# Kernel optimization log

Measured on AMD Instinct MI355X. Metric: run time of the kernel, lower is better.

## Reference

```python
import jax, jax.numpy as jnp
import numpy as np
from jax import lax

EPS = 1e-5


def setup_inputs() -> dict:
    key = jax.random.key(0)
    ks = jax.random.split(key, 8)
    b, c_in, h, w = 16, 256, 64, 64
    c_out, kh, n_exp = 512, 3, 8
    fan_in = c_in * kh * kh
    bound_w = float(np.sqrt(6.0 / fan_in))  # kaiming_uniform a=sqrt(5) -> U(-sqrt(6/fan_in), +)
    bound_b = float(1.0 / np.sqrt(fan_in))
    return {
        "x": jax.random.normal(ks[0], (b, c_in, h, w), dtype=jnp.float32),
        "expert_weight": jax.random.uniform(ks[1], (n_exp, c_out, c_in, kh, kh), jnp.float32, -bound_w, bound_w),
        "expert_bias": jax.random.uniform(ks[2], (n_exp, c_out), jnp.float32, -bound_b, bound_b),
        "fc_w": jax.random.uniform(ks[3], (n_exp, c_in), jnp.float32, -1.0 / np.sqrt(c_in), 1.0 / np.sqrt(c_in)),
        "fc_b": jax.random.uniform(ks[4], (n_exp,), jnp.float32, -1.0 / np.sqrt(c_in), 1.0 / np.sqrt(c_in)),
        "bn_gamma": jnp.ones((c_out,), jnp.float32),
        "bn_beta": jnp.zeros((c_out,), jnp.float32),
    }


def reference(x, expert_weight, expert_bias, fc_w, fc_b, bn_gamma, bn_beta):
    # --- route_func: GAP -> Linear -> sigmoid -> (b, k) ---
    pooled = x.mean(axis=(2, 3))                       # (b, c_in)
    routing = jax.nn.sigmoid(pooled @ fc_w.T + fc_b)   # (b, k)

    # --- per-sample combined kernels and biases ---
    comb_w = jnp.einsum('bk,koihw->boihw', routing, expert_weight)  # (b, c_out, c_in, kh, kw)
    comb_b = routing @ expert_bias                                  # (b, c_out)

    # --- per-sample conv (equivalent of groups=b grouped conv) ---
    def conv_one(xi, wi):
        # xi: (c_in, h, w), wi: (c_out, c_in, kh, kw)
        return lax.conv_general_dilated(
            xi[None], wi, window_strides=(1, 1), padding=[(1, 1), (1, 1)],
            rhs_dilation=(1, 1), dimension_numbers=('NCHW', 'OIHW', 'NCHW'))[0]

    out = jax.vmap(conv_one)(x, comb_w) + comb_b[:, :, None, None]  # (b, c_out, h, w)

    # --- BatchNorm2d (training mode: batch statistics) ---
    mean = out.mean(axis=(0, 2, 3))
    var = out.var(axis=(0, 2, 3))
    out = (out - mean[None, :, None, None]) * (bn_gamma * lax.rsqrt(var + EPS))[None, :, None, None] \
          + bn_beta[None, :, None, None]

    # --- LeakyReLU(0.1) ---
    return jnp.where(out > 0, out, 0.1 * out)
```

## Files before the change

### kernel.cpp

```cpp
#include <hip/hip_runtime.h>
#include <hip/hip_bf16.h>
#include <stdint.h>

typedef unsigned short u16;
typedef short bf16x8 __attribute__((ext_vector_type(8)));
typedef float f32x4 __attribute__((ext_vector_type(4)));
typedef u16 u16x8 __attribute__((ext_vector_type(8)));

#define DEVFN static __device__ __forceinline__

#define NB 16
#define CIN 256
#define HH 64
#define WW 64
#define COUT 512
#define NPX 4096
#define NSTEP 72

DEVFN u16 bf16_rne(float f){
  union { float f; uint32_t u; } v; v.f = f;
  uint32_t u = v.u;
  return (u16)((u + 0x7fffu + ((u >> 16) & 1u)) >> 16);
}

DEVFN void gload16(const void* g, void* l){
  __builtin_amdgcn_global_load_lds((const __attribute__((address_space(1))) void*)g,
                                   (__attribute__((address_space(3))) void*)l,
                                   16, 0, 0);
}

#define VMWAIT(N) asm volatile("s_waitcnt vmcnt(" #N ")" ::: "memory")
#define BARRIER() do { __builtin_amdgcn_s_barrier(); \
                       __builtin_amdgcn_sched_barrier(0); \
                       asm volatile("" ::: "memory"); } while(0)

__global__ void k_route(const float* __restrict__ pooled, const float* __restrict__ fcw,
                        const float* __restrict__ fcb, float* __restrict__ routing){
  int bk = blockIdx.x;
  int b = bk >> 3, k = bk & 7;
  int l = threadIdx.x;
  float4 pv = ((const float4*)(pooled + b*CIN))[l];
  float4 wv = ((const float4*)(fcw   + k*CIN))[l];
  float s = pv.x*wv.x + pv.y*wv.y + pv.z*wv.z + pv.w*wv.w;
  for (int o = 32; o; o >>= 1) s += __shfl_down(s, o);
  if (l == 0) routing[b*8 + k] = 1.0f / (1.0f + __expf(-(s * (1.0f/(float)NPX) + fcb[k])));
}

__global__ void k_cbias(const float* __restrict__ routing, const float* __restrict__ eb,
                        float* __restrict__ cbias){
  int idx = blockIdx.x*256 + threadIdx.x;
  int b = idx >> 9, co = idx & 511;
  float s = 0.f;
  for (int k = 0; k < 8; k++) s += routing[b*8+k] * eb[k*COUT + co];
  cbias[idx] = s;
}

__global__ void k_wcomb(const float* __restrict__ routing, const float* __restrict__ ew,
                        u16* __restrict__ wc){
  int blk  = blockIdx.x;
  int step = blk >> 6;
  int cog  = blk & 63;
  int cb = step / 9, rs = step - cb*9;
  int t = threadIdx.x;
  int ci = t & 31, co = cog*8 + (t >> 5);
  int cig = cb*32 + ci;
  float wv[8];
#pragma unroll
  for (int k = 0; k < 8; k++)
    wv[k] = ew[(size_t)((k*COUT + co)*CIN + cig)*9 + rs];
  for (int b = 0; b < NB; b++){
    float s = 0.f;
#pragma unroll
    for (int k = 0; k < 8; k++) s += routing[b*8+k] * wv[k];
    wc[((size_t)(b*NSTEP + step)*COUT + co)*32 + ci] = bf16_rne(s);
  }
}

__global__ void k_xprep(const float* __restrict__ x, u16* __restrict__ xt,
                        float* __restrict__ pooled){
  int blk = blockIdx.x;
  int ctile = blk & 3;
  int h = (blk >> 2) & 63;
  int b = blk >> 8;
  __shared__ u16 S[64][66];
  int t = threadIdx.x;
  {
    int ci_l = t >> 2, w0 = (t & 3) * 16;
    const float4* src = (const float4*)(x + ((size_t)((b*CIN + ctile*64 + ci_l)*HH + h)*WW + w0));
    float4 a = src[0], bb = src[1], c = src[2], d = src[3];
    u16* row = &S[ci_l][w0];
    row[0]=bf16_rne(a.x);  row[1]=bf16_rne(a.y);  row[2]=bf16_rne(a.z);  row[3]=bf16_rne(a.w);
    row[4]=bf16_rne(bb.x); row[5]=bf16_rne(bb.y); row[6]=bf16_rne(bb.z); row[7]=bf16_rne(bb.w);
    row[8]=bf16_rne(c.x);  row[9]=bf16_rne(c.y);  row[10]=bf16_rne(c.z); row[11]=bf16_rne(c.w);
    row[12]=bf16_rne(d.x); row[13]=bf16_rne(d.y); row[14]=bf16_rne(d.z); row[15]=bf16_rne(d.w);
    float s = a.x+a.y+a.z+a.w + bb.x+bb.y+bb.z+bb.w + c.x+c.y+c.z+c.w + d.x+d.y+d.z+d.w;
    s += __shfl_down(s, 2);
    s += __shfl_down(s, 1);
    if ((t & 3) == 0) atomicAdd(&pooled[b*CIN + ctile*64 + ci_l], s);
  }
  __syncthreads();
  {
    int w_l = t >> 2, cig = (t & 3) * 16;
    u16x8 v0, v1;
#pragma unroll
    for (int j = 0; j < 8; j++){ v0[j] = S[cig+j][w_l]; v1[j] = S[cig+8+j][w_l]; }
    u16* dst = xt + ((size_t)(b*66 + h + 1)*68 + (w_l + 1))*CIN + ctile*64 + cig;
    *(u16x8*)(dst)     = v0;
    *(u16x8*)(dst + 8) = v1;
  }
}

#define XBYTES 17408
#define WBYTES 8192

DEVFN void stage_w(const u16* __restrict__ wstep, char* dst, int wv, int l){
#pragma unroll
  for (int i = 0; i < 2; i++){
    int q = i*256 + wv*64 + l;
    int co_l = q >> 2, j = q & 3;
    gload16(wstep + co_l*32 + ((j ^ ((co_l >> 1) & 3)) << 3), dst + (i*256 + wv*64)*16);
  }
  __builtin_amdgcn_sched_barrier(0);
}

DEVFN void stage_x(const u16* __restrict__ xtb, int h0, int cioff, char* dst, int wv, int l){
#pragma unroll
  for (int i = 0; i < 5; i++){
    int qb = i*256 + wv*64;
    if (qb >= 1088) qb -= 1088;
    int q = qb + l;
    int t2 = q >> 2;
    int lr = (t2 * 964) >> 16;
    int c  = t2 - lr*68;
    int j  = q & 3;
    gload16(xtb + ((size_t)(h0 + lr)*68 + c)*CIN + cioff + ((j ^ ((c >> 1) & 3)) << 3),
            dst + qb*16);
  }
  __builtin_amdgcn_sched_barrier(0);
}

template<int RS>
DEVFN void conv_step(int cb, char* ldsbase, const char* Xc, char* Xn,
                     const u16* __restrict__ xtb, const u16* __restrict__ wcb, int h0,
                     int wv, int l, int wn, int l15, int kbq, int byteA0,
                     f32x4 acc[4][4])
{
  constexpr int r = RS / 3, s = RS - r*3;
  const char* Wc = ldsbase + (((unsigned)(cb + RS)) & 3)*WBYTES;
  char* Wp       = ldsbase + (((unsigned)(cb + RS + 3)) & 3)*WBYTES;

  int c0 = l15 + s;
  int byteB0 = ((wn + r)*68 + c0)*64 + ((kbq ^ ((c0 >> 1) & 3)) << 4);
  bf16x8 af[4], bfr[4];
#pragma unroll
  for (int m = 0; m < 4; m++) af[m]  = *(const bf16x8*)(Wc + byteA0 + m*1024);
#pragma unroll
  for (int n = 0; n < 4; n++) bfr[n] = *(const bf16x8*)(Xc + byteB0 + n*1024);

  if constexpr (RS <= 5) {
    stage_w(wcb + (size_t)(cb*9 + RS + 3)*(COUT*32), Wp, wv, l);
  } else {
    if (cb != 7) stage_w(wcb + (size_t)(cb*9 + RS + 3)*(COUT*32), Wp, wv, l);
  }
  if constexpr (RS == 4) {
    if (cb != 7) stage_x(xtb, h0, (cb+1)*32, Xn, wv, l);
  }

  if constexpr (RS <= 3)      { VMWAIT(4); BARRIER(); }
  else if constexpr (RS == 4 || RS == 5) {
    if (cb != 7) { VMWAIT(9); } else { VMWAIT(4); }
    BARRIER();
  }
  else if constexpr (RS == 6) {
    if (cb != 7) { VMWAIT(9); } else { VMWAIT(2); }
    BARRIER();
  }
  else if constexpr (RS == 7) {
    if (cb != 7) { VMWAIT(4); } else { VMWAIT(0); }
    BARRIER();
  }
  else {
    if (cb != 7) { VMWAIT(4); BARRIER(); }
  }

  __builtin_amdgcn_s_setprio(1);
#pragma unroll
  for (int m = 0; m < 4; m++)
#pragma unroll
    for (int n = 0; n < 4; n++)
      acc[m][n] = __builtin_amdgcn_mfma_f32_16x16x32_bf16(af[m], bfr[n], acc[m][n], 0, 0, 0);
  __builtin_amdgcn_s_setprio(0);
}

__global__ __launch_bounds__(256, 2) void k_conv(
    const u16* __restrict__ xt, const u16* __restrict__ wc,
    const float* __restrict__ cbias, float* __restrict__ out,
    float* __restrict__ ssum, float* __restrict__ ssq)
{
  __shared__ char lds[4*WBYTES + 2*XBYTES];
  char* Xb0 = lds + 4*WBYTES;
  char* Xb1 = lds + 4*WBYTES + XBYTES;

  int hw = blockIdx.x;
  int lb = (hw & 7) * 256 + (hw >> 3);
  int b  = lb >> 7;
  int ct = (lb >> 5) & 3;
  int pt = lb & 31;
  int h0 = pt * 2;

  int t = threadIdx.x, l = t & 63, wv = t >> 6;
  int wm = wv >> 1, wn = wv & 1;
  int l15 = l & 15, kbq = l >> 4;

  const u16* xtb = xt + (size_t)b * 66*68*CIN;
  const u16* wcb = wc + (size_t)(b*NSTEP) * COUT*32 + ct*128*32;

  f32x4 acc[4][4];
#pragma unroll
  for (int m = 0; m < 4; m++)
#pragma unroll
    for (int n = 0; n < 4; n++) acc[m][n] = (f32x4){0.f,0.f,0.f,0.f};

  const int byteA0 = (wm*64 + l15)*64 + ((kbq ^ ((l15 >> 1) & 3)) << 4);

  stage_x(xtb, h0, 0, Xb0, wv, l);
  stage_w(wcb,             lds + 0*WBYTES, wv, l);
  stage_w(wcb + COUT*32,   lds + 1*WBYTES, wv, l);
  stage_w(wcb + 2*COUT*32, lds + 2*WBYTES, wv, l);
  VMWAIT(4);
  BARRIER();

  for (int cb = 0; cb < 8; cb++){
    char* Xc = (cb & 1) ? Xb1 : Xb0;
    char* Xn = (cb & 1) ? Xb0 : Xb1;
    conv_step<0>(cb, lds, Xc,Xn, xtb,wcb,h0, wv,l,wn,l15,kbq,byteA0, acc);
    conv_step<1>(cb, lds, Xc,Xn, xtb,wcb,h0, wv,l,wn,l15,kbq,byteA0, acc);
    conv_step<2>(cb, lds, Xc,Xn, xtb,wcb,h0, wv,l,wn,l15,kbq,byteA0, acc);
    conv_step<3>(cb, lds, Xc,Xn, xtb,wcb,h0, wv,l,wn,l15,kbq,byteA0, acc);
    conv_step<4>(cb, lds, Xc,Xn, xtb,wcb,h0, wv,l,wn,l15,kbq,byteA0, acc);
    conv_step<5>(cb, lds, Xc,Xn, xtb,wcb,h0, wv,l,wn,l15,kbq,byteA0, acc);
    conv_step<6>(cb, lds, Xc,Xn, xtb,wcb,h0, wv,l,wn,l15,kbq,byteA0, acc);
    conv_step<7>(cb, lds, Xc,Xn, xtb,wcb,h0, wv,l,wn,l15,kbq,byteA0, acc);
    conv_step<8>(cb, lds, Xc,Xn, xtb,wcb,h0, wv,l,wn,l15,kbq,byteA0, acc);
  }

  int co_t = ct*128 + wm*64 + (kbq << 2);
  int px_t = pt*128 + wn*64 + l15;
  float* outb = out + (size_t)b * COUT * NPX;
#pragma unroll
  for (int m = 0; m < 4; m++){
#pragma unroll
    for (int rg = 0; rg < 4; rg++){
      int co = co_t + m*16 + rg;
      float bias = cbias[b*COUT + co];
      float s1 = 0.f, s2 = 0.f;
      size_t base = (size_t)co * NPX + px_t;
#pragma unroll
      for (int n = 0; n < 4; n++){
        float v = acc[m][n][rg] + bias;
        outb[base + n*16] = v;
        s1 += v; s2 += v*v;
      }
#pragma unroll
      for (int o = 8; o; o >>= 1){ s1 += __shfl_xor(s1, o); s2 += __shfl_xor(s2, o); }
      if (l15 == 0){ atomicAdd(&ssum[co], s1); atomicAdd(&ssq[co], s2); }
    }
  }
}

__global__ void k_stats(const float* __restrict__ ssum, const float* __restrict__ ssq,
                        const float* __restrict__ gamma, const float* __restrict__ beta,
                        float* __restrict__ sc, float* __restrict__ sh){
  int co = blockIdx.x*256 + threadIdx.x;
  const float invN = 1.0f / 65536.0f;
  float m  = ssum[co] * invN;
  float var = ssq[co] * invN - m*m;
  float scale = gamma[co] * rsqrtf(var + 1e-5f);
  sc[co] = scale;
  sh[co] = beta[co] - m*scale;
}

__global__ void k_norm(float* __restrict__ out, const float* __restrict__ sc,
                       const float* __restrict__ sh){
  const int NF4 = (NB*COUT*NPX)/4;
  int idx = blockIdx.x*256 + threadIdx.x;
  float4* o4 = (float4*)out;
  for (int i = idx; i < NF4; i += 8192*256){
    float4 v = o4[i];
    int co = (i >> 10) & 511;
    float a = sc[co], d = sh[co];
    v.x = fmaf(v.x, a, d); v.y = fmaf(v.y, a, d);
    v.z = fmaf(v.z, a, d); v.w = fmaf(v.w, a, d);
    v.x = v.x > 0.f ? v.x : 0.1f*v.x;
    v.y = v.y > 0.f ? v.y : 0.1f*v.y;
    v.z = v.z > 0.f ? v.z : 0.1f*v.z;
    v.w = v.w > 0.f ? v.w : 0.1f*v.w;
    o4[i] = v;
  }
}

extern "C" void kernel_launch(void* const* d_in, const int* in_sizes, int n_in,
                              void* d_out, int out_size, void* d_ws, size_t ws_size,
                              hipStream_t stream) {
  const float* x     = (const float*)d_in[0];
  const float* ew    = (const float*)d_in[1];
  const float* eb    = (const float*)d_in[2];
  const float* fcw   = (const float*)d_in[3];
  const float* fcb   = (const float*)d_in[4];
  const float* gamma = (const float*)d_in[5];
  const float* beta  = (const float*)d_in[6];
  float* out = (float*)d_out;

  char* ws = (char*)d_ws;
  const size_t XT_BYTES = (size_t)NB*66*68*CIN*2;
  const size_t WC_BYTES = (size_t)NB*NSTEP*COUT*32*2;
  u16* xt = (u16*)ws;
  u16* wc = (u16*)(ws + XT_BYTES);
  float* fbase   = (float*)(ws + XT_BYTES + WC_BYTES);
  float* pooled  = fbase;
  float* ssum    = fbase + 4096;
  float* ssq     = fbase + 4608;
  float* routing = fbase + 5120;
  float* cbias   = fbase + 5248;
  float* sc      = fbase + 13440;
  float* sh      = fbase + 13952;

  hipMemsetAsync(xt, 0, XT_BYTES, stream);
  hipMemsetAsync(pooled, 0, 5120*sizeof(float), stream);

  k_xprep<<<4096, 256, 0, stream>>>(x, xt, pooled);
  k_route<<<128,   64, 0, stream>>>(pooled, fcw, fcb, routing);
  k_cbias<<<32,   256, 0, stream>>>(routing, eb, cbias);
  k_wcomb<<<4608, 256, 0, stream>>>(routing, ew, wc);
  k_conv <<<2048, 256, 0, stream>>>(xt, wc, cbias, out, ssum, ssq);
  k_stats<<<2,    256, 0, stream>>>(ssum, ssq, gamma, beta, sc, sh);
  k_norm <<<8192, 256, 0, stream>>>(out, sc, sh);
}
```

Measured before the change: 313.2 us.

## Shrink conv LDS for 3 blocks/CU, store bf16 intermediate, zero only halo

The conv kernel drops from a 4-deep weight ring plus a double-buffered X tile to a 3-deep weight ring plus a single X buffer, raising launch bounds to 3 blocks per CU. The next X slice is loaded during the last tap under an extra barrier. The pre-norm conv output can now be written as bf16 to workspace and expanded by a new normalize kernel, halving intermediate traffic at some precision cost. The full xt memset is replaced by a kernel that zeroes only the padding halo, and the norm grid is reduced.

```diff
diff --git a/kernel.cpp b/kernel.cpp
--- a/kernel.cpp
+++ b/kernel.cpp
@@ -73,6 +73,21 @@
 #pragma unroll
     for (int k = 0; k < 8; k++) s += routing[b*8+k] * wv[k];
     wc[((size_t)(b*NSTEP + step)*COUT + co)*32 + ci] = bf16_rne(s);
+  }
+}
+
+__global__ void k_halo(u16* __restrict__ xt){
+  int blk = blockIdx.x;
+  int b = blk / 66, row = blk - b*66;
+  uint32_t* base = (uint32_t*)(xt + ((size_t)(b*66 + row))*68*256);
+  int t = threadIdx.x;
+  if (row == 0 || row == 65){
+    for (int i = t; i < 8704; i += 256) base[i] = 0;
+  } else {
+    for (int i = t; i < 512; i += 256){
+      int idx = (i < 128) ? i : (8320 + (i - 128));
+      base[idx] = 0;
+    }
   }
 }
 
@@ -140,14 +155,14 @@
 }
 
 template<int RS>
-DEVFN void conv_step(int cb, char* ldsbase, const char* Xc, char* Xn,
-                     const u16* __restrict__ xtb, const u16* __restrict__ wcb, int h0,
+DEVFN void conv_step(int cb, char* ldsbase, char* Xb,
+                     const u16* __restrict__ wcb,
                      int wv, int l, int wn, int l15, int kbq, int byteA0,
                      f32x4 acc[4][4])
 {
   constexpr int r = RS / 3, s = RS - r*3;
-  const char* Wc = ldsbase + (((unsigned)(cb + RS)) & 3)*WBYTES;
-  char* Wp       = ldsbase + (((unsigned)(cb + RS + 3)) & 3)*WBYTES;
+  const char* Wc = ldsbase + (RS % 3)*WBYTES;
+  char* Wp       = ldsbase + ((RS + 2) % 3)*WBYTES;
 
   int c0 = l15 + s;
   int byteB0 = ((wn + r)*68 + c0)*64 + ((kbq ^ ((c0 >> 1) & 3)) << 4);
@@ -155,33 +170,20 @@
 #pragma unroll
   for (int m = 0; m < 4; m++) af[m]  = *(const bf16x8*)(Wc + byteA0 + m*1024);
 #pragma unroll
-  for (int n = 0; n < 4; n++) bfr[n] = *(const bf16x8*)(Xc + byteB0 + n*1024);
-
-  if constexpr (RS <= 5) {
-    stage_w(wcb + (size_t)(cb*9 + RS + 3)*(COUT*32), Wp, wv, l);
+  for (int n = 0; n < 4; n++) bfr[n] = *(const bf16x8*)(Xb + byteB0 + n*1024);
+
+  if constexpr (RS <= 6) {
+    stage_w(wcb + (size_t)(cb*9 + RS + 2)*(COUT*32), Wp, wv, l);
   } else {
-    if (cb != 7) stage_w(wcb + (size_t)(cb*9 + RS + 3)*(COUT*32), Wp, wv, l);
-  }
-  if constexpr (RS == 4) {
-    if (cb != 7) stage_x(xtb, h0, (cb+1)*32, Xn, wv, l);
-  }
-
-  if constexpr (RS <= 3)      { VMWAIT(4); BARRIER(); }
-  else if constexpr (RS == 4 || RS == 5) {
-    if (cb != 7) { VMWAIT(9); } else { VMWAIT(4); }
-    BARRIER();
-  }
-  else if constexpr (RS == 6) {
-    if (cb != 7) { VMWAIT(9); } else { VMWAIT(2); }
-    BARRIER();
-  }
-  else if constexpr (RS == 7) {
-    if (cb != 7) { VMWAIT(4); } else { VMWAIT(0); }
-    BARRIER();
-  }
-  else {
-    if (cb != 7) { VMWAIT(4); BARRIER(); }
-  }
+    if (cb != 7) stage_w(wcb + (size_t)(cb*9 + RS + 2)*(COUT*32), Wp, wv, l);
+  }
+
+  if constexpr (RS == 7) {
+    if (cb == 7) { VMWAIT(0); } else { VMWAIT(2); }
+  } else {
+    VMWAIT(2);
+  }
+  BARRIER();
 
   __builtin_amdgcn_s_setprio(1);
 #pragma unroll
@@ -192,14 +194,64 @@
   __builtin_amdgcn_s_setprio(0);
 }
 
-__global__ __launch_bounds__(256, 2) void k_conv(
+DEVFN void conv_step8(int cb, char* ldsbase, char* Xb,
+                      const u16* __restrict__ xtb, const u16* __restrict__ wcb, int h0,
+                      int wv, int l, int wn, int l15, int kbq, int byteA0,
+                      f32x4 acc[4][4])
+{
+  const char* Wc = ldsbase + 2*WBYTES;
+  char* Wp       = ldsbase + 1*WBYTES;
+  int c0 = l15 + 2;
+  int byteB0 = ((wn + 2)*68 + c0)*64 + ((kbq ^ ((c0 >> 1) & 3)) << 4);
+  bf16x8 af[4], bfr[4];
+#pragma unroll
+  for (int m = 0; m < 4; m++) af[m]  = *(const bf16x8*)(Wc + byteA0 + m*1024);
+#pragma unroll
+  for (int n = 0; n < 4; n++) bfr[n] = *(const bf16x8*)(Xb + byteB0 + n*1024);
+
+  BARRIER();
+
+  stage_w(wcb + (size_t)(cb*9 + 10)*(COUT*32), Wp, wv, l);
+  stage_x(xtb, h0, (cb+1)*32, Xb, wv, l);
+
+  __builtin_amdgcn_s_setprio(1);
+#pragma unroll
+  for (int m = 0; m < 4; m++)
+#pragma unroll
+    for (int n = 0; n < 4; n++)
+      acc[m][n] = __builtin_amdgcn_mfma_f32_16x16x32_bf16(af[m], bfr[n], acc[m][n], 0, 0, 0);
+  __builtin_amdgcn_s_setprio(0);
+
+  VMWAIT(0);
+  BARRIER();
+}
+
+DEVFN void conv_step8_last(char* ldsbase, char* Xb,
+                           int wn, int l15, int kbq, int byteA0,
+                           f32x4 acc[4][4])
+{
+  const char* Wc = ldsbase + 2*WBYTES;
+  int c0 = l15 + 2;
+  int byteB0 = ((wn + 2)*68 + c0)*64 + ((kbq ^ ((c0 >> 1) & 3)) << 4);
+  bf16x8 af[4], bfr[4];
+#pragma unroll
+  for (int m = 0; m < 4; m++) af[m]  = *(const bf16x8*)(Wc + byteA0 + m*1024);
+#pragma unroll
+  for (int n = 0; n < 4; n++) bfr[n] = *(const bf16x8*)(Xb + byteB0 + n*1024);
+#pragma unroll
+  for (int m = 0; m < 4; m++)
+#pragma unroll
+    for (int n = 0; n < 4; n++)
+      acc[m][n] = __builtin_amdgcn_mfma_f32_16x16x32_bf16(af[m], bfr[n], acc[m][n], 0, 0, 0);
+}
+
+__global__ __launch_bounds__(256, 3) void k_conv(
     const u16* __restrict__ xt, const u16* __restrict__ wc,
-    const float* __restrict__ cbias, float* __restrict__ out,
+    const float* __restrict__ cbias, float* __restrict__ out, u16* __restrict__ obf,
     float* __restrict__ ssum, float* __restrict__ ssq)
 {
-  __shared__ char lds[4*WBYTES + 2*XBYTES];
-  char* Xb0 = lds + 4*WBYTES;
-  char* Xb1 = lds + 4*WBYTES + XBYTES;
+  __shared__ char lds[3*WBYTES + XBYTES];
+  char* Xb = lds + 3*WBYTES;
 
   int hw = blockIdx.x;
   int lb = (hw & 7) * 256 + (hw >> 3);
@@ -223,30 +275,27 @@
 
   const int byteA0 = (wm*64 + l15)*64 + ((kbq ^ ((l15 >> 1) & 3)) << 4);
 
-  stage_x(xtb, h0, 0, Xb0, wv, l);
-  stage_w(wcb,             lds + 0*WBYTES, wv, l);
-  stage_w(wcb + COUT*32,   lds + 1*WBYTES, wv, l);
-  stage_w(wcb + 2*COUT*32, lds + 2*WBYTES, wv, l);
-  VMWAIT(4);
+  stage_x(xtb, h0, 0, Xb, wv, l);
+  stage_w(wcb,           lds + 0*WBYTES, wv, l);
+  stage_w(wcb + COUT*32, lds + 1*WBYTES, wv, l);
+  VMWAIT(2);
   BARRIER();
 
   for (int cb = 0; cb < 8; cb++){
-    char* Xc = (cb & 1) ? Xb1 : Xb0;
-    char* Xn = (cb & 1) ? Xb0 : Xb1;
-    conv_step<0>(cb, lds, Xc,Xn, xtb,wcb,h0, wv,l,wn,l15,kbq,byteA0, acc);
-    conv_step<1>(cb, lds, Xc,Xn, xtb,wcb,h0, wv,l,wn,l15,kbq,byteA0, acc);
-    conv_step<2>(cb, lds, Xc,Xn, xtb,wcb,h0, wv,l,wn,l15,kbq,byteA0, acc);
-    conv_step<3>(cb, lds, Xc,Xn, xtb,wcb,h0, wv,l,wn,l15,kbq,byteA0, acc);
-    conv_step<4>(cb, lds, Xc,Xn, xtb,wcb,h0, wv,l,wn,l15,kbq,byteA0, acc);
-    conv_step<5>(cb, lds, Xc,Xn, xtb,wcb,h0, wv,l,wn,l15,kbq,byteA0, acc);
-    conv_step<6>(cb, lds, Xc,Xn, xtb,wcb,h0, wv,l,wn,l15,kbq,byteA0, acc);
-    conv_step<7>(cb, lds, Xc,Xn, xtb,wcb,h0, wv,l,wn,l15,kbq,byteA0, acc);
-    conv_step<8>(cb, lds, Xc,Xn, xtb,wcb,h0, wv,l,wn,l15,kbq,byteA0, acc);
+    conv_step<0>(cb, lds, Xb, wcb, wv,l,wn,l15,kbq,byteA0, acc);
+    conv_step<1>(cb, lds, Xb, wcb, wv,l,wn,l15,kbq,byteA0, acc);
+    conv_step<2>(cb, lds, Xb, wcb, wv,l,wn,l15,kbq,byteA0, acc);
+    conv_step<3>(cb, lds, Xb, wcb, wv,l,wn,l15,kbq,byteA0, acc);
+    conv_step<4>(cb, lds, Xb, wcb, wv,l,wn,l15,kbq,byteA0, acc);
+    conv_step<5>(cb, lds, Xb, wcb, wv,l,wn,l15,kbq,byteA0, acc);
+    conv_step<6>(cb, lds, Xb, wcb, wv,l,wn,l15,kbq,byteA0, acc);
+    conv_step<7>(cb, lds, Xb, wcb, wv,l,wn,l15,kbq,byteA0, acc);
+    if (cb < 7) conv_step8(cb, lds, Xb, xtb, wcb, h0, wv,l,wn,l15,kbq,byteA0, acc);
+    else        conv_step8_last(lds, Xb, wn,l15,kbq,byteA0, acc);
   }
 
   int co_t = ct*128 + wm*64 + (kbq << 2);
   int px_t = pt*128 + wn*64 + l15;
-  float* outb = out + (size_t)b * COUT * NPX;
 #pragma unroll
   for (int m = 0; m < 4; m++){
 #pragma unroll
@@ -254,11 +303,12 @@
       int co = co_t + m*16 + rg;
       float bias = cbias[b*COUT + co];
       float s1 = 0.f, s2 = 0.f;
-      size_t base = (size_t)co * NPX + px_t;
+      size_t base = ((size_t)b * COUT + co) * NPX + px_t;
 #pragma unroll
       for (int n = 0; n < 4; n++){
         float v = acc[m][n][rg] + bias;
-        outb[base + n*16] = v;
+        if (obf) obf[base + n*16] = bf16_rne(v);
+        else     out[base + n*16] = v;
         s1 += v; s2 += v*v;
       }
 #pragma unroll
@@ -285,7 +335,7 @@
   const int NF4 = (NB*COUT*NPX)/4;
   int idx = blockIdx.x*256 + threadIdx.x;
   float4* o4 = (float4*)out;
-  for (int i = idx; i < NF4; i += 8192*256){
+  for (int i = idx; i < NF4; i += 2048*256){
     float4 v = o4[i];
     int co = (i >> 10) & 511;
     float a = sc[co], d = sh[co];
@@ -296,6 +346,27 @@
     v.z = v.z > 0.f ? v.z : 0.1f*v.z;
     v.w = v.w > 0.f ? v.w : 0.1f*v.w;
     o4[i] = v;
+  }
+}
+
+__global__ void k_norm_bf16(const u16* __restrict__ obf, float* __restrict__ out,
+                            const float* __restrict__ sc, const float* __restrict__ sh){
+  const int NG = (NB*COUT*NPX)/8;
+  int idx = blockIdx.x*256 + threadIdx.x;
+  for (int g = idx; g < NG; g += 2048*256){
+    u16x8 v = *(const u16x8*)(obf + (size_t)g*8);
+    int co = (g >> 9) & 511;
+    float a = sc[co], d = sh[co];
+    float vv[8];
+#pragma unroll
+    for (int j = 0; j < 8; j++){
+      union{ uint32_t u; float f; } c; c.u = ((uint32_t)(u16)v[j]) << 16;
+      float w = fmaf(c.f, a, d);
+      vv[j] = w > 0.f ? w : 0.1f*w;
+    }
+    float4* o4 = (float4*)(out + (size_t)g*8);
+    o4[0] = (float4){vv[0],vv[1],vv[2],vv[3]};
+    o4[1] = (float4){vv[4],vv[5],vv[6],vv[7]};
   }
 }
 
@@ -312,8 +383,10 @@
   float* out = (float*)d_out;
 
   char* ws = (char*)d_ws;
-  const size_t XT_BYTES = (size_t)NB*66*68*CIN*2;
-  const size_t WC_BYTES = (size_t)NB*NSTEP*COUT*32*2;
+  const size_t XT_BYTES  = (size_t)NB*66*68*CIN*2;
+  const size_t WC_BYTES  = (size_t)NB*NSTEP*COUT*32*2;
+  const size_t FL_BYTES  = 65536;
+  const size_t OBF_BYTES = (size_t)NB*COUT*NPX*2;
   u16* xt = (u16*)ws;
   u16* wc = (u16*)(ws + XT_BYTES);
   float* fbase   = (float*)(ws + XT_BYTES + WC_BYTES);
@@ -324,15 +397,18 @@
   float* cbias   = fbase + 5248;
   float* sc      = fbase + 13440;
   float* sh      = fbase + 13952;
-
-  hipMemsetAsync(xt, 0, XT_BYTES, stream);
+  bool use_bf16 = ws_size >= XT_BYTES + WC_BYTES + FL_BYTES + OBF_BYTES;
+  u16* obf = use_bf16 ? (u16*)(ws + XT_BYTES + WC_BYTES + FL_BYTES) : (u16*)nullptr;
+
   hipMemsetAsync(pooled, 0, 5120*sizeof(float), stream);
 
+  k_halo <<<1056, 256, 0, stream>>>(xt);
   k_xprep<<<4096, 256, 0, stream>>>(x, xt, pooled);
   k_route<<<128,   64, 0, stream>>>(pooled, fcw, fcb, routing);
   k_cbias<<<32,   256, 0, stream>>>(routing, eb, cbias);
   k_wcomb<<<4608, 256, 0, stream>>>(routing, ew, wc);
-  k_conv <<<2048, 256, 0, stream>>>(xt, wc, cbias, out, ssum, ssq);
+  k_conv <<<2048, 256, 0, stream>>>(xt, wc, cbias, out, obf, ssum, ssq);
   k_stats<<<2,    256, 0, stream>>>(ssum, ssq, gamma, beta, sc, sh);
-  k_norm <<<8192, 256, 0, stream>>>(out, sc, sh);
-}
+  if (use_bf16) k_norm_bf16<<<2048, 256, 0, stream>>>(obf, out, sc, sh);
+  else          k_norm     <<<2048, 256, 0, stream>>>(out, sc, sh);
+}
```

Result: no change. 311.6 us (-0.5%).
